# Kernel optimization log

Hardware: AMD Instinct MI355X
Metric: run time of the kernel (lower is better)

Reference implementation:

```python
import jax, jax.numpy as jnp
import numpy as np
import math

D_MODEL, N_HEADS, D_HEAD = 1024, 16, 64
INIT_RANGE = 0.02
IGNORE = -100000.0


def setup_inputs() -> dict:
    key = jax.random.key(0)
    ks = jax.random.split(key, 5)
    x = jax.random.normal(ks[0], (2, 2048, D_MODEL), dtype=jnp.float32)
    W_Q = INIT_RANGE * jax.random.normal(ks[1], (N_HEADS, D_MODEL, D_HEAD), dtype=jnp.float32)
    W_K = INIT_RANGE * jax.random.normal(ks[2], (N_HEADS, D_MODEL, D_HEAD), dtype=jnp.float32)
    W_V = INIT_RANGE * jax.random.normal(ks[3], (N_HEADS, D_MODEL, D_HEAD), dtype=jnp.float32)
    # W_O is contracted as 'n_heads d_head d_model' in the original einsum
    W_O = INIT_RANGE * jax.random.normal(ks[4], (N_HEADS, D_HEAD, D_MODEL), dtype=jnp.float32)
    b_Q = jnp.zeros((N_HEADS, D_HEAD), dtype=jnp.float32)
    b_K = jnp.zeros((N_HEADS, D_HEAD), dtype=jnp.float32)
    b_V = jnp.zeros((N_HEADS, D_HEAD), dtype=jnp.float32)
    b_O = jnp.zeros((D_MODEL,), dtype=jnp.float32)
    return {"normalized_resid_pre": x, "W_Q": W_Q, "b_Q": b_Q, "W_K": W_K, "b_K": b_K,
            "W_V": W_V, "b_V": b_V, "W_O": W_O, "b_O": b_O}


def reference(normalized_resid_pre, W_Q, b_Q, W_K, b_K, W_V, b_V, W_O, b_O):
    x = normalized_resid_pre  # [b, s, d_model]
    q = jnp.einsum('bsd,hde->bshe', x, W_Q) + b_Q  # [b, s, h, d_head]
    k = jnp.einsum('bsd,hde->bshe', x, W_K) + b_K
    v = jnp.einsum('bsd,hde->bshe', x, W_V) + b_V
    scores = jnp.einsum('bqhe,bkhe->bhqk', q, k) / math.sqrt(D_HEAD)
    S = x.shape[1]
    causal = jnp.tril(jnp.ones((S, S), dtype=bool))  # True where allowed
    scores = jnp.where(causal, scores, IGNORE)
    pattern = jax.nn.softmax(scores, axis=-1)  # [b, h, q, k]
    z = jnp.einsum('bhqk,bkhe->bqhe', pattern, v)
    attn_out = jnp.einsum('bqhe,hed->bqd', z, W_O) + b_O
    return attn_out
```

## Files before the change

### kernel.cpp

```cpp
#include <hip/hip_runtime.h>
#include <cstdint>
#include <cstddef>

typedef unsigned short u16;
typedef __bf16 bf16x8 __attribute__((ext_vector_type(8)));
typedef _Float16 f16x4 __attribute__((ext_vector_type(4)));
typedef _Float16 f16x2 __attribute__((ext_vector_type(2)));
typedef float  f32x4  __attribute__((ext_vector_type(4)));
typedef unsigned short u16x8 __attribute__((ext_vector_type(8)));
typedef unsigned short u16x4 __attribute__((ext_vector_type(4)));

#define DM   1024
#define NH   16
#define DH   64
#define SS   2048
#define BSZ  4096
#define NQKV 3072
#define QSCALE 0.18033688011f

__device__ __forceinline__ u16 f2b(float f) {
  unsigned u = __builtin_bit_cast(unsigned, f);
  return (u16)((u + 0x7FFFu + ((u >> 16) & 1u)) >> 16);
}
__device__ __forceinline__ u16 f2h(float f) {
  _Float16 h = (_Float16)f;
  return __builtin_bit_cast(u16, h);
}

__device__ __forceinline__ void gl_lds16(const void* g, void* l) {
  __builtin_amdgcn_global_load_lds(
      (__attribute__((address_space(1))) void*)(void*)g,
      (__attribute__((address_space(3))) void*)l, 16, 0, 0);
}

__global__ __launch_bounds__(256) void prep_all_kernel(
    const float* __restrict__ x, u16* __restrict__ xb,
    const float* __restrict__ Wq, const float* __restrict__ Wk,
    const float* __restrict__ Wv, u16* __restrict__ wqkvt,
    const float* __restrict__ Wo, u16* __restrict__ wot) {
  __shared__ __align__(16) u16 Ts[64 * 72];
  int bid = blockIdx.x, t = threadIdx.x;
  if (bid < 2048) {
    int i = (bid * 256 + t) * 8;
    float4 a = *(const float4*)(x + i);
    float4 b = *(const float4*)(x + i + 4);
    u16x8 o;
    o[0] = f2b(a.x); o[1] = f2b(a.y); o[2] = f2b(a.z); o[3] = f2b(a.w);
    o[4] = f2b(b.x); o[5] = f2b(b.y); o[6] = f2b(b.z); o[7] = f2b(b.w);
    *(u16x8*)(xb + i) = o;
    return;
  }
  if (bid < 2816) {
    int idx = bid - 2048;
    int dt = idx & 15, sl = idx >> 4;
    int proj = sl >> 4, h = sl & 15;
    const float* W = (proj == 0) ? Wq : ((proj == 1) ? Wk : Wv);
    int d0 = dt * 64;
    {
      int ld = t >> 2;
      int ec = (t & 3) * 16;
      const float* src = W + ((size_t)h * DM + d0 + ld) * DH + ec;
      float4 v0 = *(const float4*)(src);
      float4 v1 = *(const float4*)(src + 4);
      float4 v2 = *(const float4*)(src + 8);
      float4 v3 = *(const float4*)(src + 12);
      float vv[16] = {v0.x, v0.y, v0.z, v0.w, v1.x, v1.y, v1.z, v1.w,
                      v2.x, v2.y, v2.z, v2.w, v3.x, v3.y, v3.z, v3.w};
#pragma unroll
      for (int i = 0; i < 16; i++) Ts[(ec + i) * 72 + ld] = f2b(vv[i]);
    }
    __syncthreads();
    {
      int le = t >> 2;
      int dc = (t & 3) * 16;
      int n = proj * DM + h * DH + le;
      u16* dst = wqkvt + (size_t)n * DM + d0 + dc;
      *(u16x8*)(dst)     = *(const u16x8*)&Ts[le * 72 + dc];
      *(u16x8*)(dst + 8) = *(const u16x8*)&Ts[le * 72 + dc + 8];
    }
    return;
  }
  {
    int idx = bid - 2816;
    int dt = idx & 15, h = idx >> 4;
    int d0 = dt * 64;
    {
      int le = t >> 2;
      int dc = (t & 3) * 16;
      const float* src = Wo + ((size_t)h * DH + le) * DM + d0 + dc;
      float4 v0 = *(const float4*)(src);
      float4 v1 = *(const float4*)(src + 4);
      float4 v2 = *(const float4*)(src + 8);
      float4 v3 = *(const float4*)(src + 12);
      float vv[16] = {v0.x, v0.y, v0.z, v0.w, v1.x, v1.y, v1.z, v1.w,
                      v2.x, v2.y, v2.z, v2.w, v3.x, v3.y, v3.z, v3.w};
#pragma unroll
      for (int i = 0; i < 16; i++) Ts[(dc + i) * 72 + le] = f2b(vv[i]);
    }
    __syncthreads();
    {
      int ld = t >> 2;
      int ec = (t & 3) * 16;
      u16* dst = wot + (size_t)(d0 + ld) * DM + h * DH + ec;
      *(u16x8*)(dst)     = *(const u16x8*)&Ts[ld * 72 + ec];
      *(u16x8*)(dst + 8) = *(const u16x8*)&Ts[ld * 72 + ec + 8];
    }
  }
}

__global__ __launch_bounds__(256) void transpose_v_kernel(const u16* __restrict__ v,
                                                          u16* __restrict__ vt) {
  __shared__ __align__(16) u16 Ts[64 * 72];
  int t = threadIdx.x;
  int st = blockIdx.x;
  int bh = blockIdx.y;
  int s0 = st * 64;
  {
    int ls = t >> 2;
    int ec = (t & 3) * 16;
    const u16* src = v + ((size_t)bh * SS + s0 + ls) * DH + ec;
    u16x8 a0 = *(const u16x8*)src;
    u16x8 a1 = *(const u16x8*)(src + 8);
#pragma unroll
    for (int i = 0; i < 8; i++) Ts[(ec + i) * 72 + ls] = a0[i];
#pragma unroll
    for (int i = 0; i < 8; i++) Ts[(ec + 8 + i) * 72 + ls] = a1[i];
  }
  __syncthreads();
  {
    int le = t >> 2;
    int sc = (t & 3) * 16;
    u16* dst = vt + ((size_t)bh * DH + le) * SS + s0 + sc;
    *(u16x8*)(dst)     = *(const u16x8*)&Ts[le * 72 + sc];
    *(u16x8*)(dst + 8) = *(const u16x8*)&Ts[le * 72 + sc + 8];
  }
}

__global__ __launch_bounds__(256) void gemm_qkv_kernel(
    const u16* __restrict__ A, const u16* __restrict__ Bt,
    u16* __restrict__ o_q, u16* __restrict__ o_k, u16* __restrict__ o_v,
    const float* __restrict__ c0, const float* __restrict__ c1,
    const float* __restrict__ c2) {
  const int K = DM;
  __shared__ __align__(16) u16 As[128 * 32];
  __shared__ __align__(16) u16 Bs[128 * 32];
  int t = threadIdx.x, w = t >> 6, l = t & 63;
  int lr = l & 15, lq = l >> 4;
  int m0 = blockIdx.x * 128, n0 = blockIdx.y * 128;
  int wr = w >> 1, wc = w & 1;
  f32x4 acc[4][4] = {};
  const u16* ga = A + (size_t)(m0 + (t >> 2)) * K + (t & 3) * 8;
  const u16* gb = Bt + (size_t)(n0 + (t >> 2)) * K + (t & 3) * 8;

  for (int k0 = 0; k0 < K; k0 += 32) {
    __syncthreads();
    gl_lds16(ga + k0,           &As[w * 512]);
    gl_lds16(ga + k0 + 64 * K,  &As[2048 + w * 512]);
    gl_lds16(gb + k0,           &Bs[w * 512]);
    gl_lds16(gb + k0 + 64 * K,  &Bs[2048 + w * 512]);
    __syncthreads();
    bf16x8 af[4], bfr[4];
#pragma unroll
    for (int i = 0; i < 4; i++)
      af[i] = *(const bf16x8*)&As[(wr * 64 + i * 16 + lr) * 32 + lq * 8];
#pragma unroll
    for (int j = 0; j < 4; j++)
      bfr[j] = *(const bf16x8*)&Bs[(wc * 64 + j * 16 + lr) * 32 + lq * 8];
#pragma unroll
    for (int i = 0; i < 4; i++)
#pragma unroll
      for (int j = 0; j < 4; j++)
        acc[i][j] = __builtin_amdgcn_mfma_f32_16x16x32_bf16(af[i], bfr[j], acc[i][j], 0, 0, 0);
  }

  int mb = m0 + wr * 64 + lq * 4;
  int nb = n0 + wc * 64 + lr;
#pragma unroll
  for (int j = 0; j < 4; j++) {
    int n = nb + j * 16;
    int proj = n >> 10, r = n & 1023;
    int h = r >> 6, e = r & 63;
    const float* bp = (proj == 0) ? c0 : ((proj == 1) ? c1 : c2);
    float bias = bp[r];
#pragma unroll
    for (int i = 0; i < 4; i++) {
#pragma unroll
      for (int g = 0; g < 4; g++) {
        int m = mb + i * 16 + g;
        int b = m >> 11, s = m & 2047;
        float val = acc[i][j][g] + bias;
        size_t bhh = (size_t)(b * NH + h);
        if (proj == 0)      o_q[(bhh * SS + s) * DH + e] = f2b(val * QSCALE);
        else if (proj == 1) o_k[(bhh * SS + s) * DH + e] = f2b(val);
        else                o_v[(bhh * SS + s) * DH + e] = f2h(val);
      }
    }
  }
}

__global__ __launch_bounds__(256) void gemm_o_kernel(
    const u16* __restrict__ A, const u16* __restrict__ Bt,
    const float* __restrict__ bo, float* __restrict__ fout) {
  const int K = DM;
  __shared__ __align__(16) u16 As[128 * 32];
  __shared__ __align__(16) u16 Bs[64 * 32];
  int t = threadIdx.x, w = t >> 6, l = t & 63;
  int lr = l & 15, lq = l >> 4;
  int m0 = blockIdx.x * 128, n0 = blockIdx.y * 64;
  f32x4 acc[2][4] = {};
  const u16* ga = A + (size_t)(m0 + (t >> 2)) * K + (t & 3) * 8;
  const u16* gb = Bt + (size_t)(n0 + (t >> 2)) * K + (t & 3) * 8;

  for (int k0 = 0; k0 < K; k0 += 32) {
    __syncthreads();
    gl_lds16(ga + k0,           &As[w * 512]);
    gl_lds16(ga + k0 + 64 * K,  &As[2048 + w * 512]);
    if (t < 256) gl_lds16(gb + k0, &Bs[w * 512]);
    __syncthreads();
    bf16x8 af[2], bfr[4];
#pragma unroll
    for (int i = 0; i < 2; i++)
      af[i] = *(const bf16x8*)&As[(w * 32 + i * 16 + lr) * 32 + lq * 8];
#pragma unroll
    for (int j = 0; j < 4; j++)
      bfr[j] = *(const bf16x8*)&Bs[(j * 16 + lr) * 32 + lq * 8];
#pragma unroll
    for (int i = 0; i < 2; i++)
#pragma unroll
      for (int j = 0; j < 4; j++)
        acc[i][j] = __builtin_amdgcn_mfma_f32_16x16x32_bf16(af[i], bfr[j], acc[i][j], 0, 0, 0);
  }

  int mb = m0 + w * 32 + lq * 4;
  int nb = n0 + lr;
#pragma unroll
  for (int j = 0; j < 4; j++) {
    int n = nb + j * 16;
    float bias = bo[n];
#pragma unroll
    for (int i = 0; i < 2; i++) {
#pragma unroll
      for (int g = 0; g < 4; g++) {
        int m = mb + i * 16 + g;
        fout[(size_t)m * DM + n] = acc[i][j][g] + bias;
      }
    }
  }
}

__global__ __launch_bounds__(256) void attn_kernel(const u16* __restrict__ q_ws,
                                                   const u16* __restrict__ k_ws,
                                                   const u16* __restrict__ vt_ws,
                                                   u16* __restrict__ z_ws) {
  __shared__ __align__(16) u16 Ks[2][64 * 72];
  __shared__ __align__(16) u16 Vs[2][64 * 72];
  int t = threadIdx.x, w = t >> 6, l = t & 63;
  int lr = l & 15, lq = l >> 4;
  int bid = blockIdx.x;
  int xcd = bid & 7, idx = bid >> 3;
  int bh = xcd * 4 + (idx & 3);
  int j = idx >> 2;
  const u16* Qb = q_ws + (size_t)bh * SS * DH;
  const u16* Kb = k_ws + (size_t)bh * SS * DH;
  const u16* Vb = vt_ws + (size_t)bh * DH * SS;
  int b = bh >> 4, h = bh & 15;

  const f16x4 ones = {(_Float16)1.f, (_Float16)1.f, (_Float16)1.f, (_Float16)1.f};

  int srow = t >> 3;
  int sc8 = (t & 7) * 8;

  for (int half = 0; half < 2; half++) {
    int qt = half ? (31 - j) : j;
    int q0 = qt * 64;
    int nkt = qt + 1;

    int qrow = q0 + w * 16 + lr;
    bf16x8 qf0 = *(const bf16x8*)(Qb + (size_t)qrow * DH + lq * 8);
    bf16x8 qf1 = *(const bf16x8*)(Qb + (size_t)qrow * DH + 32 + lq * 8);

    f32x4 accO[4] = {};
    f32x4 accL = {};
    float mrow = -1e30f;

    __syncthreads();
    {
      const u16* kg = Kb + (size_t)srow * DH + sc8;
      const u16* vg = Vb + (size_t)srow * SS + sc8;
      u16x8 r0 = *(const u16x8*)kg;
      u16x8 r1 = *(const u16x8*)(kg + 32 * DH);
      u16x8 r2 = *(const u16x8*)vg;
      u16x8 r3 = *(const u16x8*)(vg + 32 * SS);
      *(u16x8*)&Ks[0][srow * 72 + sc8] = r0;
      *(u16x8*)&Ks[0][(srow + 32) * 72 + sc8] = r1;
      *(u16x8*)&Vs[0][srow * 72 + sc8] = r2;
      *(u16x8*)&Vs[0][(srow + 32) * 72 + sc8] = r3;
    }

    for (int kt = 0; kt < nkt; ++kt) {
      __syncthreads();
      int pb = kt & 1;

      u16x8 r0, r1, r2, r3;
      bool have_next = (kt + 1 < nkt);
      if (have_next) {
        int k0n = (kt + 1) * 64;
        const u16* kg = Kb + (size_t)(k0n + srow) * DH + sc8;
        const u16* vg = Vb + (size_t)srow * SS + k0n + sc8;
        r0 = *(const u16x8*)kg;
        r1 = *(const u16x8*)(kg + 32 * DH);
        r2 = *(const u16x8*)vg;
        r3 = *(const u16x8*)(vg + 32 * SS);
      }

      f32x4 sc[4];
#pragma unroll
      for (int nt = 0; nt < 4; nt++) {
        bf16x8 kf0 = *(const bf16x8*)&Ks[pb][(nt * 16 + lr) * 72 + lq * 8];
        bf16x8 kf1 = *(const bf16x8*)&Ks[pb][(nt * 16 + lr) * 72 + 32 + lq * 8];
        f32x4 a = {0.f, 0.f, 0.f, 0.f};
        a = __builtin_amdgcn_mfma_f32_16x16x32_bf16(kf0, qf0, a, 0, 0, 0);
        a = __builtin_amdgcn_mfma_f32_16x16x32_bf16(kf1, qf1, a, 0, 0, 0);
        sc[nt] = a;
      }

      if (kt == nkt - 1) {
        int k0 = kt * 64;
        int gq = q0 + w * 16 + lr;
#pragma unroll
        for (int nt = 0; nt < 4; nt++) {
#pragma unroll
          for (int g = 0; g < 4; g++) {
            int gk = k0 + nt * 16 + lq * 4 + g;
            if (gk > gq) sc[nt][g] = -1e30f;
          }
        }
      }

      float mt = -1e30f;
#pragma unroll
      for (int nt = 0; nt < 4; nt++)
#pragma unroll
        for (int g = 0; g < 4; g++) mt = fmaxf(mt, sc[nt][g]);
      mt = fmaxf(mt, __shfl_xor(mt, 16));
      mt = fmaxf(mt, __shfl_xor(mt, 32));

      if (__any(mt > mrow)) {
        float mn = fmaxf(mrow, mt);
        float alpha = exp2f(mrow - mn);
        mrow = mn;
#pragma unroll
        for (int g = 0; g < 4; g++) accL[g] *= alpha;
#pragma unroll
        for (int et = 0; et < 4; et++)
#pragma unroll
          for (int g = 0; g < 4; g++) accO[et][g] *= alpha;
      }

      f16x4 pf[4];
#pragma unroll
      for (int nt = 0; nt < 4; nt++) {
        float p0 = exp2f(sc[nt][0] - mrow);
        float p1 = exp2f(sc[nt][1] - mrow);
        float p2 = exp2f(sc[nt][2] - mrow);
        float p3 = exp2f(sc[nt][3] - mrow);
        f16x2 e0 = __builtin_bit_cast(f16x2, __builtin_amdgcn_cvt_pkrtz(p0, p1));
        f16x2 e1 = __builtin_bit_cast(f16x2, __builtin_amdgcn_cvt_pkrtz(p2, p3));
        pf[nt][0] = e0[0]; pf[nt][1] = e0[1];
        pf[nt][2] = e1[0]; pf[nt][3] = e1[1];
      }

#pragma unroll
      for (int ks = 0; ks < 4; ks++) {
        accL = __builtin_amdgcn_mfma_f32_16x16x16f16(ones, pf[ks], accL, 0, 0, 0);
#pragma unroll
        for (int et = 0; et < 4; et++) {
          f16x4 vf = *(const f16x4*)&Vs[pb][(et * 16 + lr) * 72 + ks * 16 + lq * 4];
          accO[et] = __builtin_amdgcn_mfma_f32_16x16x16f16(vf, pf[ks], accO[et], 0, 0, 0);
        }
      }

      if (have_next) {
        int nb2 = (kt + 1) & 1;
        *(u16x8*)&Ks[nb2][srow * 72 + sc8] = r0;
        *(u16x8*)&Ks[nb2][(srow + 32) * 72 + sc8] = r1;
        *(u16x8*)&Vs[nb2][srow * 72 + sc8] = r2;
        *(u16x8*)&Vs[nb2][(srow + 32) * 72 + sc8] = r3;
      }
    }

    float inv = 1.0f / accL[0];
    int gq = q0 + w * 16 + lr;
    u16* zrow = z_ws + ((size_t)(b * SS + gq)) * DM + h * DH;
#pragma unroll
    for (int et = 0; et < 4; et++) {
      u16x4 o;
#pragma unroll
      for (int g = 0; g < 4; g++) o[g] = f2b(accO[et][g] * inv);
      *(u16x4*)(zrow + et * 16 + lq * 4) = o;
    }
  }
}

extern "C" void kernel_launch(void* const* d_in, const int* in_sizes, int n_in,
                              void* d_out, int out_size, void* d_ws, size_t ws_size,
                              hipStream_t stream) {
  const float* x  = (const float*)d_in[0];
  const float* Wq = (const float*)d_in[1];
  const float* bq = (const float*)d_in[2];
  const float* Wk = (const float*)d_in[3];
  const float* bk = (const float*)d_in[4];
  const float* Wv = (const float*)d_in[5];
  const float* bv = (const float*)d_in[6];
  const float* Wo = (const float*)d_in[7];
  const float* bo = (const float*)d_in[8];
  float* out = (float*)d_out;

  char* ws = (char*)d_ws;
  const size_t MB = 1u << 20;
  u16* xb    = (u16*)(ws);
  u16* wqkvt = (u16*)(ws + 8 * MB);
  u16* wot   = (u16*)(ws + 14 * MB);
  u16* q_ws  = (u16*)(ws + 16 * MB);
  u16* k_ws  = (u16*)(ws + 24 * MB);
  u16* v_ws  = (u16*)(ws + 32 * MB);
  u16* vt_ws = (u16*)(ws + 40 * MB);
  u16* z_ws  = (u16*)(ws + 48 * MB);

  prep_all_kernel<<<3072, 256, 0, stream>>>(x, xb, Wq, Wk, Wv, wqkvt, Wo, wot);

  gemm_qkv_kernel<<<dim3(BSZ / 128, NQKV / 128), 256, 0, stream>>>(
      xb, wqkvt, q_ws, k_ws, v_ws, bq, bk, bv);

  transpose_v_kernel<<<dim3(32, 32), 256, 0, stream>>>(v_ws, vt_ws);

  attn_kernel<<<512, 256, 0, stream>>>(q_ws, k_ws, vt_ws, z_ws);

  gemm_o_kernel<<<dim3(BSZ / 128, DM / 64), 256, 0, stream>>>(z_ws, wot, bo, out);
}
```

Baseline: 201.3 us.

## Split attention KV range across two thread groups with cross-group softmax merge

The attention block grows to 512 threads, split into two 256-thread groups. Each group processes half of the causal KV tiles for the same query tile, with its own double-buffered shared memory. The partial max, sum and output accumulators are then merged through shared memory before the bf16 output is written. The aim is to shorten the serial KV loop per block and raise parallelism per CU. The cost is extra LDS, more barriers, idle iterations in group 0 when the tile count is odd, and a merge step.

```diff
diff --git a/kernel.cpp b/kernel.cpp
--- a/kernel.cpp
+++ b/kernel.cpp
@@ -248,14 +248,26 @@
   }
 }
 
-__global__ __launch_bounds__(256) void attn_kernel(const u16* __restrict__ q_ws,
+__global__ __launch_bounds__(512) void attn_kernel(const u16* __restrict__ q_ws,
                                                    const u16* __restrict__ k_ws,
                                                    const u16* __restrict__ vt_ws,
                                                    u16* __restrict__ z_ws) {
-  __shared__ __align__(16) u16 Ks[2][64 * 72];
-  __shared__ __align__(16) u16 Vs[2][64 * 72];
-  int t = threadIdx.x, w = t >> 6, l = t & 63;
+  __shared__ __align__(16) u16 KsA[2][64 * 72], VsA[2][64 * 72];
+  __shared__ __align__(16) u16 KsB[2][64 * 72], VsB[2][64 * 72];
+  __shared__ float mlbuf[2][64][2];
+
+  int t = threadIdx.x;
+  int g = t >> 8;
+  int tl = t & 255;
+  int w4 = tl >> 6;
+  int l = t & 63;
   int lr = l & 15, lq = l >> 4;
+  int srow = tl >> 3;
+  int sc8 = (tl & 7) * 8;
+
+  u16 (*Ks)[64 * 72] = g ? KsB : KsA;
+  u16 (*Vs)[64 * 72] = g ? VsB : VsA;
+
   int bid = blockIdx.x;
   int xcd = bid & 7, idx = bid >> 3;
   int bh = xcd * 4 + (idx & 3);
@@ -263,19 +275,20 @@
   const u16* Qb = q_ws + (size_t)bh * SS * DH;
   const u16* Kb = k_ws + (size_t)bh * SS * DH;
   const u16* Vb = vt_ws + (size_t)bh * DH * SS;
-  int b = bh >> 4, h = bh & 15;
+  int b = bh >> 4, h16 = bh & 15;
 
   const f16x4 ones = {(_Float16)1.f, (_Float16)1.f, (_Float16)1.f, (_Float16)1.f};
-
-  int srow = t >> 3;
-  int sc8 = (t & 7) * 8;
 
   for (int half = 0; half < 2; half++) {
     int qt = half ? (31 - j) : j;
     int q0 = qt * 64;
     int nkt = qt + 1;
-
-    int qrow = q0 + w * 16 + lr;
+    int h = nkt >> 1;
+    int cnt1 = nkt - h;
+    int mycnt = g ? cnt1 : h;
+    int base = g ? h : 0;
+
+    int qrow = q0 + w4 * 16 + lr;
     bf16x8 qf0 = *(const bf16x8*)(Qb + (size_t)qrow * DH + lq * 8);
     bf16x8 qf1 = *(const bf16x8*)(Qb + (size_t)qrow * DH + 32 + lq * 8);
 
@@ -284,9 +297,10 @@
     float mrow = -1e30f;
 
     __syncthreads();
-    {
-      const u16* kg = Kb + (size_t)srow * DH + sc8;
-      const u16* vg = Vb + (size_t)srow * SS + sc8;
+    if (mycnt > 0) {
+      int k0 = base * 64;
+      const u16* kg = Kb + (size_t)(k0 + srow) * DH + sc8;
+      const u16* vg = Vb + (size_t)srow * SS + k0 + sc8;
       u16x8 r0 = *(const u16x8*)kg;
       u16x8 r1 = *(const u16x8*)(kg + 32 * DH);
       u16x8 r2 = *(const u16x8*)vg;
@@ -297,14 +311,15 @@
       *(u16x8*)&Vs[0][(srow + 32) * 72 + sc8] = r3;
     }
 
-    for (int kt = 0; kt < nkt; ++kt) {
+    for (int it = 0; it < cnt1; ++it) {
       __syncthreads();
-      int pb = kt & 1;
+      bool act = it < mycnt;
+      int pb = it & 1;
 
       u16x8 r0, r1, r2, r3;
-      bool have_next = (kt + 1 < nkt);
+      bool have_next = (it + 1 < mycnt);
       if (have_next) {
-        int k0n = (kt + 1) * 64;
+        int k0n = (base + it + 1) * 64;
         const u16* kg = Kb + (size_t)(k0n + srow) * DH + sc8;
         const u16* vg = Vb + (size_t)srow * SS + k0n + sc8;
         r0 = *(const u16x8*)kg;
@@ -313,75 +328,77 @@
         r3 = *(const u16x8*)(vg + 32 * SS);
       }
 
-      f32x4 sc[4];
-#pragma unroll
-      for (int nt = 0; nt < 4; nt++) {
-        bf16x8 kf0 = *(const bf16x8*)&Ks[pb][(nt * 16 + lr) * 72 + lq * 8];
-        bf16x8 kf1 = *(const bf16x8*)&Ks[pb][(nt * 16 + lr) * 72 + 32 + lq * 8];
-        f32x4 a = {0.f, 0.f, 0.f, 0.f};
-        a = __builtin_amdgcn_mfma_f32_16x16x32_bf16(kf0, qf0, a, 0, 0, 0);
-        a = __builtin_amdgcn_mfma_f32_16x16x32_bf16(kf1, qf1, a, 0, 0, 0);
-        sc[nt] = a;
-      }
-
-      if (kt == nkt - 1) {
-        int k0 = kt * 64;
-        int gq = q0 + w * 16 + lr;
+      if (act) {
+        f32x4 sc[4];
 #pragma unroll
         for (int nt = 0; nt < 4; nt++) {
-#pragma unroll
-          for (int g = 0; g < 4; g++) {
-            int gk = k0 + nt * 16 + lq * 4 + g;
-            if (gk > gq) sc[nt][g] = -1e30f;
+          bf16x8 kf0 = *(const bf16x8*)&Ks[pb][(nt * 16 + lr) * 72 + lq * 8];
+          bf16x8 kf1 = *(const bf16x8*)&Ks[pb][(nt * 16 + lr) * 72 + 32 + lq * 8];
+          f32x4 a = {0.f, 0.f, 0.f, 0.f};
+          a = __builtin_amdgcn_mfma_f32_16x16x32_bf16(kf0, qf0, a, 0, 0, 0);
+          a = __builtin_amdgcn_mfma_f32_16x16x32_bf16(kf1, qf1, a, 0, 0, 0);
+          sc[nt] = a;
+        }
+
+        if (g == 1 && it == cnt1 - 1) {
+          int k0 = (base + it) * 64;
+          int gq = q0 + w4 * 16 + lr;
+#pragma unroll
+          for (int nt = 0; nt < 4; nt++) {
+#pragma unroll
+            for (int gg = 0; gg < 4; gg++) {
+              int gk = k0 + nt * 16 + lq * 4 + gg;
+              if (gk > gq) sc[nt][gg] = -1e30f;
+            }
           }
         }
-      }
-
-      float mt = -1e30f;
-#pragma unroll
-      for (int nt = 0; nt < 4; nt++)
-#pragma unroll
-        for (int g = 0; g < 4; g++) mt = fmaxf(mt, sc[nt][g]);
-      mt = fmaxf(mt, __shfl_xor(mt, 16));
-      mt = fmaxf(mt, __shfl_xor(mt, 32));
-
-      if (__any(mt > mrow)) {
-        float mn = fmaxf(mrow, mt);
-        float alpha = exp2f(mrow - mn);
-        mrow = mn;
-#pragma unroll
-        for (int g = 0; g < 4; g++) accL[g] *= alpha;
-#pragma unroll
-        for (int et = 0; et < 4; et++)
-#pragma unroll
-          for (int g = 0; g < 4; g++) accO[et][g] *= alpha;
-      }
-
-      f16x4 pf[4];
-#pragma unroll
-      for (int nt = 0; nt < 4; nt++) {
-        float p0 = exp2f(sc[nt][0] - mrow);
-        float p1 = exp2f(sc[nt][1] - mrow);
-        float p2 = exp2f(sc[nt][2] - mrow);
-        float p3 = exp2f(sc[nt][3] - mrow);
-        f16x2 e0 = __builtin_bit_cast(f16x2, __builtin_amdgcn_cvt_pkrtz(p0, p1));
-        f16x2 e1 = __builtin_bit_cast(f16x2, __builtin_amdgcn_cvt_pkrtz(p2, p3));
-        pf[nt][0] = e0[0]; pf[nt][1] = e0[1];
-        pf[nt][2] = e1[0]; pf[nt][3] = e1[1];
-      }
-
-#pragma unroll
-      for (int ks = 0; ks < 4; ks++) {
-        accL = __builtin_amdgcn_mfma_f32_16x16x16f16(ones, pf[ks], accL, 0, 0, 0);
-#pragma unroll
-        for (int et = 0; et < 4; et++) {
-          f16x4 vf = *(const f16x4*)&Vs[pb][(et * 16 + lr) * 72 + ks * 16 + lq * 4];
-          accO[et] = __builtin_amdgcn_mfma_f32_16x16x16f16(vf, pf[ks], accO[et], 0, 0, 0);
+
+        float mt = -1e30f;
+#pragma unroll
+        for (int nt = 0; nt < 4; nt++)
+#pragma unroll
+          for (int gg = 0; gg < 4; gg++) mt = fmaxf(mt, sc[nt][gg]);
+        mt = fmaxf(mt, __shfl_xor(mt, 16));
+        mt = fmaxf(mt, __shfl_xor(mt, 32));
+
+        if (__any(mt > mrow)) {
+          float mn = fmaxf(mrow, mt);
+          float alpha = exp2f(mrow - mn);
+          mrow = mn;
+#pragma unroll
+          for (int gg = 0; gg < 4; gg++) accL[gg] *= alpha;
+#pragma unroll
+          for (int et = 0; et < 4; et++)
+#pragma unroll
+            for (int gg = 0; gg < 4; gg++) accO[et][gg] *= alpha;
+        }
+
+        f16x4 pf[4];
+#pragma unroll
+        for (int nt = 0; nt < 4; nt++) {
+          float p0 = exp2f(sc[nt][0] - mrow);
+          float p1 = exp2f(sc[nt][1] - mrow);
+          float p2 = exp2f(sc[nt][2] - mrow);
+          float p3 = exp2f(sc[nt][3] - mrow);
+          f16x2 e0 = __builtin_bit_cast(f16x2, __builtin_amdgcn_cvt_pkrtz(p0, p1));
+          f16x2 e1 = __builtin_bit_cast(f16x2, __builtin_amdgcn_cvt_pkrtz(p2, p3));
+          pf[nt][0] = e0[0]; pf[nt][1] = e0[1];
+          pf[nt][2] = e1[0]; pf[nt][3] = e1[1];
+        }
+
+#pragma unroll
+        for (int ks = 0; ks < 4; ks++) {
+          accL = __builtin_amdgcn_mfma_f32_16x16x16f16(ones, pf[ks], accL, 0, 0, 0);
+#pragma unroll
+          for (int et = 0; et < 4; et++) {
+            f16x4 vf = *(const f16x4*)&Vs[pb][(et * 16 + lr) * 72 + ks * 16 + lq * 4];
+            accO[et] = __builtin_amdgcn_mfma_f32_16x16x16f16(vf, pf[ks], accO[et], 0, 0, 0);
+          }
         }
       }
 
       if (have_next) {
-        int nb2 = (kt + 1) & 1;
+        int nb2 = (it + 1) & 1;
         *(u16x8*)&Ks[nb2][srow * 72 + sc8] = r0;
         *(u16x8*)&Ks[nb2][(srow + 32) * 72 + sc8] = r1;
         *(u16x8*)&Vs[nb2][srow * 72 + sc8] = r2;
@@ -389,15 +406,49 @@
       }
     }
 
-    float inv = 1.0f / accL[0];
-    int gq = q0 + w * 16 + lr;
-    u16* zrow = z_ws + ((size_t)(b * SS + gq)) * DM + h * DH;
-#pragma unroll
-    for (int et = 0; et < 4; et++) {
-      u16x4 o;
-#pragma unroll
-      for (int g = 0; g < 4; g++) o[g] = f2b(accO[et][g] * inv);
-      *(u16x4*)(zrow + et * 16 + lq * 4) = o;
+    __syncthreads();
+    if (lq == 0) {
+      mlbuf[g][w4 * 16 + lr][0] = mrow;
+      mlbuf[g][w4 * 16 + lr][1] = accL[0];
+    }
+    __syncthreads();
+    float mo = mlbuf[1 - g][w4 * 16 + lr][0];
+    float lo = mlbuf[1 - g][w4 * 16 + lr][1];
+    float m  = fmaxf(mrow, mo);
+    float alpha = exp2f(mrow - m);
+    float lsum  = alpha * accL[0] + exp2f(mo - m) * lo;
+    float inv   = 1.0f / lsum;
+
+    float* cbuf = (float*)VsB[1];
+    int gq = q0 + w4 * 16 + lr;
+    int crow = w4 * 16 + lr;
+    u16* zrow = z_ws + ((size_t)(b * SS + gq)) * DM + h16 * DH;
+#pragma unroll
+    for (int c = 0; c < 2; c++) {
+      if (g == 1) {
+#pragma unroll
+        for (int e2 = 0; e2 < 2; e2++) {
+          int et = 2 * c + e2;
+#pragma unroll
+          for (int gg = 0; gg < 4; gg++)
+            cbuf[crow * 32 + e2 * 16 + lq * 4 + gg] = alpha * accO[et][gg];
+        }
+      }
+      __syncthreads();
+      if (g == 0) {
+#pragma unroll
+        for (int e2 = 0; e2 < 2; e2++) {
+          int et = 2 * c + e2;
+          u16x4 o;
+#pragma unroll
+          for (int gg = 0; gg < 4; gg++) {
+            float v = alpha * accO[et][gg] + cbuf[crow * 32 + e2 * 16 + lq * 4 + gg];
+            o[gg] = f2b(v * inv);
+          }
+          *(u16x4*)(zrow + et * 16 + lq * 4) = o;
+        }
+      }
+      __syncthreads();
     }
   }
 }
@@ -434,7 +485,7 @@
 
   transpose_v_kernel<<<dim3(32, 32), 256, 0, stream>>>(v_ws, vt_ws);
 
-  attn_kernel<<<512, 256, 0, stream>>>(q_ws, k_ws, vt_ws, z_ws);
+  attn_kernel<<<512, 512, 0, stream>>>(q_ws, k_ws, vt_ws, z_ws);
 
   gemm_o_kernel<<<dim3(BSZ / 128, DM / 64), 256, 0, stream>>>(z_ws, wot, bo, out);
 }
```

New measurement: 195.3 us. 1.03x faster.
